# Performance work log

Hardware: AMD Instinct MI355X
Metric: run time of the kernel (lower is better)

The kernel has to match this reference:

```python
import jax, jax.numpy as jnp
import numpy as np

D_MODEL = 1024
N_HEAD = 16
DK = D_MODEL // N_HEAD
NEG = -10000.0  # module uses masked_fill with -10000.0, not -inf


def setup_inputs() -> dict:
    key = jax.random.key(0)
    k1, k2, k3 = jax.random.split(key, 3)
    B, T = 8, 1024
    x = jax.random.normal(k1, (B, T, D_MODEL), dtype=jnp.float32)
    # torch Linear(d, 3d, bias=False): y = x @ W.T with W [3d, d]; store transposed
    w_qkv = jax.random.normal(k2, (D_MODEL, 3 * D_MODEL), dtype=jnp.float32) * (1.0 / np.sqrt(D_MODEL))
    w_proj = jax.random.normal(k3, (D_MODEL, D_MODEL), dtype=jnp.float32) * (1.0 / np.sqrt(D_MODEL))
    return {"x": x, "w_qkv": w_qkv, "w_proj": w_proj}


def reference(x, w_qkv, w_proj):
    B, T, C = x.shape
    qkv = x @ w_qkv  # [B, T, 3C]
    q, k, v = jnp.split(qkv, 3, axis=-1)
    # [B, H, T, dk]
    q = q.reshape(B, T, N_HEAD, DK).transpose(0, 2, 1, 3)
    k = k.reshape(B, T, N_HEAD, DK).transpose(0, 2, 1, 3)
    v = v.reshape(B, T, N_HEAD, DK).transpose(0, 2, 1, 3)
    att = jnp.einsum('bhqd,bhkd->bhqk', q, k) / jnp.sqrt(jnp.float32(DK))
    causal = jnp.tril(jnp.ones((T, T), dtype=bool))  # [T, T]
    att = jnp.where(causal[None, None], att, NEG)
    att = jax.nn.softmax(att, axis=-1)
    y = jnp.einsum('bhqk,bhkd->bhqd', att, v)  # [B, H, T, dk]
    y = y.transpose(0, 2, 1, 3).reshape(B, T, C)
    return y @ w_proj
```

## Files before the change

kernel.cpp:

```cpp
#include <hip/hip_runtime.h>

typedef short bf16x8 __attribute__((ext_vector_type(8)));
typedef float f32x4 __attribute__((ext_vector_type(4)));
typedef unsigned u32x4 __attribute__((ext_vector_type(4)));

__device__ __forceinline__ unsigned short f2bf(float f) {
  unsigned u = __builtin_bit_cast(unsigned, f);
  u += 0x7fff + ((u >> 16) & 1);
  return (unsigned short)(u >> 16);
}

__device__ __forceinline__ void gload_lds16(const void* g, void* l) {
  __builtin_amdgcn_global_load_lds(
      (const __attribute__((address_space(1))) void*)g,
      (__attribute__((address_space(3))) void*)l, 16, 0, 0);
}

__global__ __launch_bounds__(256) void prep(const float* __restrict__ x,
                                            const float* __restrict__ wqkv,
                                            const float* __restrict__ wproj,
                                            unsigned short* __restrict__ xb,
                                            unsigned short* __restrict__ wqkvT,
                                            unsigned short* __restrict__ wprojT) {
  __shared__ float tile[32][33];
  const int tid = threadIdx.x;
  const int bid = blockIdx.x;
  if (bid < 2048) {
    int i = bid * 256 + tid;
    const int stride = 2048 * 256;
    for (; i < 2097152; i += stride) {
      float4 v = ((const float4*)x)[i];
      ushort4 o;
      o.x = f2bf(v.x); o.y = f2bf(v.y); o.z = f2bf(v.z); o.w = f2bf(v.w);
      ((ushort4*)xb)[i] = o;
    }
    return;
  }
  const float* in;
  unsigned short* out;
  int R, C, c0, r0;
  if (bid < 5120) {
    int b = bid - 2048;
    in = wqkv; out = wqkvT; R = 1024; C = 3072;
    c0 = (b % 96) * 32; r0 = (b / 96) * 32;
  } else {
    int b = bid - 5120;
    in = wproj; out = wprojT; R = 1024; C = 1024;
    c0 = (b % 32) * 32; r0 = (b / 32) * 32;
  }
  const int tr = tid >> 3;
  const int tc4 = tid & 7;
  float4 v = *(const float4*)&in[(size_t)(r0 + tr) * C + c0 + tc4 * 4];
  tile[tr][tc4 * 4 + 0] = v.x;
  tile[tr][tc4 * 4 + 1] = v.y;
  tile[tr][tc4 * 4 + 2] = v.z;
  tile[tr][tc4 * 4 + 3] = v.w;
  __syncthreads();
#pragma unroll
  for (int i = 0; i < 4; ++i)
    out[(size_t)(c0 + tr) * R + r0 + tc4 * 4 + i] = f2bf(tile[tc4 * 4 + i][tr]);
}

__global__ __launch_bounds__(256) void transpV(const unsigned short* __restrict__ qkv,
                                               unsigned short* __restrict__ vT) {
  const int tt = blockIdx.x, bh = blockIdx.y;
  const int b = bh >> 4, h = bh & 15;
  __shared__ unsigned short tile[64 * 64];
  const int tid = threadIdx.x;
  const size_t gbase = (size_t)b * 1024 * 3072 + 2048 + (size_t)h * 64;
#pragma unroll
  for (int i = 0; i < 2; ++i) {
    int c = i * 256 + tid;
    int trow = c >> 3, dc = c & 7;
    *(uint4*)(&tile[c * 8]) =
        *(const uint4*)(qkv + gbase + (size_t)(tt * 64 + trow) * 3072 + dc * 8);
  }
  __syncthreads();
  const int d = tid & 63, th = tid >> 6;
  unsigned short buf[16];
#pragma unroll
  for (int j = 0; j < 16; ++j) buf[j] = tile[(th * 16 + j) * 64 + d];
  size_t obase = ((size_t)bh * 64 + d) * 1024 + tt * 64 + th * 16;
  *(uint4*)(&vT[obase]) = *(uint4*)(&buf[0]);
  *(uint4*)(&vT[obase + 8]) = *(uint4*)(&buf[8]);
}

template <int OUT_BF16>
__global__ __launch_bounds__(256) void gemm_bt(const unsigned short* __restrict__ A,
                                               const unsigned short* __restrict__ B,
                                               void* __restrict__ Cv,
                                               int M, int N, int K, int lda) {
  __shared__ unsigned short As[128 * 64];
  __shared__ unsigned short Bs[128 * 64];
  const int tid = threadIdx.x;
  const int wv = tid >> 6, lane = tid & 63;
  const int l15 = lane & 15, lg = lane >> 4;
  const int bm = blockIdx.y, bn = blockIdx.x;
  const int wr = wv >> 1, wc = wv & 1;
  f32x4 acc[4][4] = {};
  const unsigned short* Ab = A + (size_t)bm * 128 * lda;
  const unsigned short* Bb = B + (size_t)bn * 128 * K;

  for (int k0 = 0; k0 < K; k0 += 64) {
#pragma unroll
    for (int i = 0; i < 4; ++i) {
      int s = i * 256 + wv * 64 + lane;
      int row = s >> 3, pc = s & 7;
      int lc = pc ^ (row & 7);
      gload_lds16(Ab + (size_t)row * lda + k0 + lc * 8,
                  (char*)As + (size_t)(i * 256 + wv * 64) * 16);
      gload_lds16(Bb + (size_t)row * K + k0 + lc * 8,
                  (char*)Bs + (size_t)(i * 256 + wv * 64) * 16);
    }
    __syncthreads();
#pragma unroll
    for (int kh = 0; kh < 2; ++kh) {
      bf16x8 af[4], bf[4];
#pragma unroll
      for (int m = 0; m < 4; ++m) {
        int row = wr * 64 + m * 16 + l15;
        int pc = (kh * 4 + lg) ^ (row & 7);
        af[m] = *(const bf16x8*)((const char*)As + (row * 8 + pc) * 16);
      }
#pragma unroll
      for (int n = 0; n < 4; ++n) {
        int row = wc * 64 + n * 16 + l15;
        int pc = (kh * 4 + lg) ^ (row & 7);
        bf[n] = *(const bf16x8*)((const char*)Bs + (row * 8 + pc) * 16);
      }
#pragma unroll
      for (int m = 0; m < 4; ++m)
#pragma unroll
        for (int n = 0; n < 4; ++n)
          acc[m][n] = __builtin_amdgcn_mfma_f32_16x16x32_bf16(af[m], bf[n], acc[m][n], 0, 0, 0);
    }
    __syncthreads();
  }

  const int rbase = bm * 128 + wr * 64;
  const int cbase = bn * 128 + wc * 64;
#pragma unroll
  for (int m = 0; m < 4; ++m)
#pragma unroll
    for (int n = 0; n < 4; ++n)
#pragma unroll
      for (int r = 0; r < 4; ++r) {
        int row = rbase + m * 16 + lg * 4 + r;
        int col = cbase + n * 16 + l15;
        float v = acc[m][n][r];
        if (OUT_BF16)
          ((unsigned short*)Cv)[(size_t)row * N + col] = f2bf(v);
        else
          ((float*)Cv)[(size_t)row * N + col] = v;
      }
}

__global__ __launch_bounds__(256) void attn_fwd(const unsigned short* __restrict__ qkv,
                                                const unsigned short* __restrict__ vT,
                                                unsigned short* __restrict__ qkv_y) {
  const int bh = blockIdx.x;
  const int pair = blockIdx.y;
  const int b = bh >> 4, h = bh & 15;
  const int tid = threadIdx.x;
  const int wv = tid >> 6, lane = tid & 63;
  const int l15 = lane & 15, lg = lane >> 4;

  __shared__ unsigned short Ks[2][64 * 64];
  __shared__ unsigned short Vs[2][64 * 64];

  const size_t base = (size_t)b * 1024 * 3072;
  const float CSCL = 0.18033688f;
  const int kq = wv * 16 + l15;

  const int idx0 = (l15 + ((lg & 1) << 5)) << 2;
  const int idx1 = idx0 + 64;
  const bool hi_nt = (lg & 2) != 0;

#pragma unroll
  for (int phase = 0; phase < 2; ++phase) {
    const int qt = phase ? 15 - pair : pair;
    const int q0 = qt * 64;
    const int qrow = q0 + wv * 16 + l15;
    const int rowg_base = q0 + wv * 16 + lg * 4;

    bf16x8 qa[2];
#pragma unroll
    for (int kh = 0; kh < 2; ++kh)
      qa[kh] = *(const bf16x8*)(qkv + base + (size_t)qrow * 3072 + h * 64 + kh * 32 + lg * 8);

    float l_sum = 0.f;
    f32x4 oacc[4] = {};

#pragma unroll
    for (int i = 0; i < 2; ++i) {
      int s = i * 256 + wv * 64 + lane;
      int row = s >> 3, pc = s & 7;
      int lc = pc ^ (row & 7);
      gload_lds16(qkv + base + (size_t)row * 3072 + 1024 + h * 64 + lc * 8,
                  (char*)(&Ks[0][0]) + (size_t)s * 16);
      gload_lds16(vT + ((size_t)bh * 64 + row) * 1024 + lc * 8,
                  (char*)(&Vs[0][0]) + (size_t)s * 16);
    }
    __syncthreads();

    for (int t = 0; t <= qt; ++t) {
      const int cur = t & 1;
      if (t < qt) {
        const int kv1 = (t + 1) * 64;
#pragma unroll
        for (int i = 0; i < 2; ++i) {
          int s = i * 256 + wv * 64 + lane;
          int row = s >> 3, pc = s & 7;
          int lc = pc ^ (row & 7);
          gload_lds16(qkv + base + (size_t)(kv1 + row) * 3072 + 1024 + h * 64 + lc * 8,
                      (char*)(&Ks[cur ^ 1][0]) + (size_t)s * 16);
          gload_lds16(vT + ((size_t)bh * 64 + row) * 1024 + kv1 + lc * 8,
                      (char*)(&Vs[cur ^ 1][0]) + (size_t)s * 16);
        }
      }

      f32x4 sacc[4] = {};
#pragma unroll
      for (int kh = 0; kh < 2; ++kh) {
        bf16x8 kf[4];
#pragma unroll
        for (int nt = 0; nt < 4; ++nt) {
          int row = nt * 16 + l15;
          int pc = (kh * 4 + lg) ^ (row & 7);
          kf[nt] = *(const bf16x8*)((const char*)(&Ks[cur][0]) + (row * 8 + pc) * 16);
        }
#pragma unroll
        for (int nt = 0; nt < 4; ++nt)
          sacc[nt] = __builtin_amdgcn_mfma_f32_16x16x32_bf16(kf[nt], qa[kh], sacc[nt], 0, 0, 0);
      }

      const bool diag = (t == qt);
      float sv[4][4];
#pragma unroll
      for (int nt = 0; nt < 4; ++nt)
#pragma unroll
        for (int r = 0; r < 4; ++r) {
          float s = sacc[nt][r] * CSCL;
          if (diag && (nt * 16 + lg * 4 + r > kq)) s = -1e30f;
          sv[nt][r] = exp2f(s);
        }

      {
        float ts = 0.f;
#pragma unroll
        for (int nt = 0; nt < 4; ++nt)
#pragma unroll
          for (int r = 0; r < 4; ++r) ts += sv[nt][r];
        ts += __shfl_xor(ts, 16);
        ts += __shfl_xor(ts, 32);
        l_sum += ts;
      }

      unsigned P2[4][2];
#pragma unroll
      for (int nt = 0; nt < 4; ++nt)
#pragma unroll
        for (int i = 0; i < 2; ++i)
          asm("v_cvt_pk_bf16_f32 %0, %1, %2"
              : "=v"(P2[nt][i]) : "v"(sv[nt][2 * i]), "v"(sv[nt][2 * i + 1]));

      u32x4 paw0, paw1;
#pragma unroll
      for (int w = 0; w < 4; ++w) {
        int idx = (w & 2) ? idx1 : idx0;
        int ri = w & 1;
        unsigned a0 = (unsigned)__builtin_amdgcn_ds_bpermute(idx, (int)P2[0][ri]);
        unsigned b0 = (unsigned)__builtin_amdgcn_ds_bpermute(idx, (int)P2[1][ri]);
        paw0[w] = hi_nt ? b0 : a0;
        unsigned a1 = (unsigned)__builtin_amdgcn_ds_bpermute(idx, (int)P2[2][ri]);
        unsigned b1 = (unsigned)__builtin_amdgcn_ds_bpermute(idx, (int)P2[3][ri]);
        paw1[w] = hi_nt ? b1 : a1;
      }
      bf16x8 pa[2];
      pa[0] = __builtin_bit_cast(bf16x8, paw0);
      pa[1] = __builtin_bit_cast(bf16x8, paw1);

#pragma unroll
      for (int kh = 0; kh < 2; ++kh)
#pragma unroll
        for (int nt = 0; nt < 4; ++nt) {
          int row = nt * 16 + l15;
          int pc = (kh * 4 + lg) ^ (row & 7);
          bf16x8 vf = *(const bf16x8*)((const char*)(&Vs[cur][0]) + (row * 8 + pc) * 16);
          oacc[nt] = __builtin_amdgcn_mfma_f32_16x16x32_bf16(pa[kh], vf, oacc[nt], 0, 0, 0);
        }
      __syncthreads();
    }

    float linv[4];
#pragma unroll
    for (int r = 0; r < 4; ++r) {
      int q = lg * 4 + r;
      float lv = __builtin_bit_cast(
          float, __builtin_amdgcn_ds_bpermute(q << 2, __builtin_bit_cast(int, l_sum)));
      linv[r] = 1.0f / lv;
    }

#pragma unroll
    for (int nt = 0; nt < 4; ++nt) {
#pragma unroll
      for (int r = 0; r < 4; ++r) {
        int row = rowg_base + r;
        int col = h * 64 + nt * 16 + l15;
        qkv_y[((size_t)b * 1024 + row) * 3072 + 2048 + col] = f2bf(oacc[nt][r] * linv[r]);
      }
    }
    __syncthreads();
  }
}

extern "C" void kernel_launch(void* const* d_in, const int* in_sizes, int n_in,
                              void* d_out, int out_size, void* d_ws, size_t ws_size,
                              hipStream_t stream) {
  const float* x = (const float*)d_in[0];
  const float* w_qkv = (const float*)d_in[1];
  const float* w_proj = (const float*)d_in[2];

  unsigned short* xb     = (unsigned short*)d_ws;
  unsigned short* vT     = (unsigned short*)d_ws;
  unsigned short* wqkvT  = (unsigned short*)((char*)d_ws + (16u << 20));
  unsigned short* wprojT = (unsigned short*)((char*)d_ws + (22u << 20));
  unsigned short* qkvb   = (unsigned short*)((char*)d_ws + (24u << 20));

  prep<<<6144, 256, 0, stream>>>(x, w_qkv, w_proj, xb, wqkvT, wprojT);

  gemm_bt<1><<<dim3(24, 64), 256, 0, stream>>>(xb, wqkvT, qkvb, 8192, 3072, 1024, 1024);

  transpV<<<dim3(16, 128), 256, 0, stream>>>(qkvb, vT);

  attn_fwd<<<dim3(128, 8), 256, 0, stream>>>(qkvb, vT, qkvb);

  gemm_bt<0><<<dim3(8, 64), 256, 0, stream>>>(qkvb + 2048, wprojT, d_out, 8192, 1024, 1024, 3072);
}
```

Measured before the change: 230.3 us.

## Triple-buffer GEMM K-tiles with async LDS loads and register prefetch

Replaces the single-buffered GEMM, which used a 64-wide K tile and two barriers per step, with a three-slot LDS ring of 32-wide K tiles. Global-to-LDS loads are issued ahead of use, and fragments for the next tile are read into registers while MFMAs run on the current one. There is now one barrier per step, plus manual waitcnt/sched_barrier control and setprio around the MFMA block. The aim is to hide global memory latency behind compute. In exchange the XOR swizzle is dropped, which may cause LDS bank conflicts, and each barrier now covers fewer MFMAs.

```diff
diff --git a/kernel.cpp b/kernel.cpp
--- a/kernel.cpp
+++ b/kernel.cpp
@@ -86,12 +86,12 @@
 }
 
 template <int OUT_BF16>
-__global__ __launch_bounds__(256) void gemm_bt(const unsigned short* __restrict__ A,
-                                               const unsigned short* __restrict__ B,
-                                               void* __restrict__ Cv,
-                                               int M, int N, int K, int lda) {
-  __shared__ unsigned short As[128 * 64];
-  __shared__ unsigned short Bs[128 * 64];
+__global__ __launch_bounds__(256, 3) void gemm_p3(const unsigned short* __restrict__ A,
+                                                  const unsigned short* __restrict__ B,
+                                                  void* __restrict__ Cv,
+                                                  int M, int N, int K, int lda) {
+  __shared__ unsigned short As[3][128 * 32];
+  __shared__ unsigned short Bs[3][128 * 32];
   const int tid = threadIdx.x;
   const int wv = tid >> 6, lane = tid & 63;
   const int l15 = lane & 15, lg = lane >> 4;
@@ -100,42 +100,66 @@
   f32x4 acc[4][4] = {};
   const unsigned short* Ab = A + (size_t)bm * 128 * lda;
   const unsigned short* Bb = B + (size_t)bn * 128 * K;
-
-  for (int k0 = 0; k0 < K; k0 += 64) {
-#pragma unroll
-    for (int i = 0; i < 4; ++i) {
+  const int NT = K >> 5;
+
+  auto STAGE = [&](int t) {
+    int slot = t % 3;
+#pragma unroll
+    for (int i = 0; i < 2; ++i) {
       int s = i * 256 + wv * 64 + lane;
-      int row = s >> 3, pc = s & 7;
-      int lc = pc ^ (row & 7);
-      gload_lds16(Ab + (size_t)row * lda + k0 + lc * 8,
-                  (char*)As + (size_t)(i * 256 + wv * 64) * 16);
-      gload_lds16(Bb + (size_t)row * K + k0 + lc * 8,
-                  (char*)Bs + (size_t)(i * 256 + wv * 64) * 16);
-    }
-    __syncthreads();
-#pragma unroll
-    for (int kh = 0; kh < 2; ++kh) {
-      bf16x8 af[4], bf[4];
-#pragma unroll
-      for (int m = 0; m < 4; ++m) {
-        int row = wr * 64 + m * 16 + l15;
-        int pc = (kh * 4 + lg) ^ (row & 7);
-        af[m] = *(const bf16x8*)((const char*)As + (row * 8 + pc) * 16);
-      }
-#pragma unroll
-      for (int n = 0; n < 4; ++n) {
-        int row = wc * 64 + n * 16 + l15;
-        int pc = (kh * 4 + lg) ^ (row & 7);
-        bf[n] = *(const bf16x8*)((const char*)Bs + (row * 8 + pc) * 16);
-      }
-#pragma unroll
-      for (int m = 0; m < 4; ++m)
-#pragma unroll
-        for (int n = 0; n < 4; ++n)
-          acc[m][n] = __builtin_amdgcn_mfma_f32_16x16x32_bf16(af[m], bf[n], acc[m][n], 0, 0, 0);
-    }
-    __syncthreads();
-  }
+      int row = s >> 2, cc = s & 3;
+      gload_lds16(Ab + (size_t)row * lda + t * 32 + cc * 8,
+                  (char*)(&As[slot][0]) + (size_t)(i * 256 + wv * 64) * 16);
+      gload_lds16(Bb + (size_t)row * K + t * 32 + cc * 8,
+                  (char*)(&Bs[slot][0]) + (size_t)(i * 256 + wv * 64) * 16);
+    }
+  };
+
+  bf16x8 af[4], bf[4];
+
+  STAGE(0); STAGE(1); STAGE(2);
+  asm volatile("s_waitcnt vmcnt(4)" ::: "memory");
+  __builtin_amdgcn_s_barrier();
+#pragma unroll
+  for (int m = 0; m < 4; ++m)
+    af[m] = *(const bf16x8*)(&As[0][0] + (wr * 64 + m * 16 + l15) * 32 + lg * 8);
+#pragma unroll
+  for (int n = 0; n < 4; ++n)
+    bf[n] = *(const bf16x8*)(&Bs[0][0] + (wc * 64 + n * 16 + l15) * 32 + lg * 8);
+  asm volatile("s_waitcnt lgkmcnt(0)" ::: "memory");
+  __builtin_amdgcn_sched_barrier(0);
+  __builtin_amdgcn_s_barrier();
+  __builtin_amdgcn_sched_barrier(0);
+
+  for (int t = 0; t < NT; ++t) {
+    __builtin_amdgcn_s_setprio(1);
+#pragma unroll
+    for (int m = 0; m < 4; ++m)
+#pragma unroll
+      for (int n = 0; n < 4; ++n)
+        acc[m][n] = __builtin_amdgcn_mfma_f32_16x16x32_bf16(af[m], bf[n], acc[m][n], 0, 0, 0);
+    __builtin_amdgcn_s_setprio(0);
+    if (t == NT - 1) break;
+
+    const unsigned short* as = &As[(t + 1) % 3][0];
+    const unsigned short* bs = &Bs[(t + 1) % 3][0];
+#pragma unroll
+    for (int m = 0; m < 4; ++m)
+      af[m] = *(const bf16x8*)(as + (wr * 64 + m * 16 + l15) * 32 + lg * 8);
+#pragma unroll
+    for (int n = 0; n < 4; ++n)
+      bf[n] = *(const bf16x8*)(bs + (wc * 64 + n * 16 + l15) * 32 + lg * 8);
+
+    STAGE(t + 3 < NT ? t + 3 : NT - 1);
+
+    asm volatile("s_waitcnt vmcnt(4)" ::: "memory");
+    asm volatile("s_waitcnt lgkmcnt(0)" ::: "memory");
+    __builtin_amdgcn_sched_barrier(0);
+    __builtin_amdgcn_s_barrier();
+    __builtin_amdgcn_sched_barrier(0);
+  }
+
+  asm volatile("s_waitcnt vmcnt(0)" ::: "memory");
 
   const int rbase = bm * 128 + wr * 64;
   const int cbase = bn * 128 + wc * 64;
@@ -329,11 +353,11 @@
 
   prep<<<6144, 256, 0, stream>>>(x, w_qkv, w_proj, xb, wqkvT, wprojT);
 
-  gemm_bt<1><<<dim3(24, 64), 256, 0, stream>>>(xb, wqkvT, qkvb, 8192, 3072, 1024, 1024);
+  gemm_p3<1><<<dim3(24, 64), 256, 0, stream>>>(xb, wqkvT, qkvb, 8192, 3072, 1024, 1024);
 
   transpV<<<dim3(16, 128), 256, 0, stream>>>(qkvb, vT);
 
   attn_fwd<<<dim3(128, 8), 256, 0, stream>>>(qkvb, vT, qkvb);
 
-  gemm_bt<0><<<dim3(8, 64), 256, 0, stream>>>(qkvb + 2048, wprojT, d_out, 8192, 1024, 1024, 3072);
-}
+  gemm_p3<0><<<dim3(8, 64), 256, 0, stream>>>(qkvb + 2048, wprojT, d_out, 8192, 1024, 1024, 3072);
+}
```

Result: slower. 239.3 us (+3.9%).

## Compute V transposed via swapped-operand GEMM and drop transpose kernel

Applied to the files above, without the earlier changes.

Splits the QKV projection into a Q/K GEMM and a separate GEMM that computes V already transposed by swapping operands. This removes the standalone V transpose kernel and its extra read and write of V. Attention addressing and workspace layout are updated, and the attention output now lives in a compact buffer for the output projection. It adds one more GEMM launch with a different tile shape.

```diff
diff --git a/kernel.cpp b/kernel.cpp
--- a/kernel.cpp
+++ b/kernel.cpp
@@ -61,30 +61,6 @@
     out[(size_t)(c0 + tr) * R + r0 + tc4 * 4 + i] = f2bf(tile[tc4 * 4 + i][tr]);
 }
 
-__global__ __launch_bounds__(256) void transpV(const unsigned short* __restrict__ qkv,
-                                               unsigned short* __restrict__ vT) {
-  const int tt = blockIdx.x, bh = blockIdx.y;
-  const int b = bh >> 4, h = bh & 15;
-  __shared__ unsigned short tile[64 * 64];
-  const int tid = threadIdx.x;
-  const size_t gbase = (size_t)b * 1024 * 3072 + 2048 + (size_t)h * 64;
-#pragma unroll
-  for (int i = 0; i < 2; ++i) {
-    int c = i * 256 + tid;
-    int trow = c >> 3, dc = c & 7;
-    *(uint4*)(&tile[c * 8]) =
-        *(const uint4*)(qkv + gbase + (size_t)(tt * 64 + trow) * 3072 + dc * 8);
-  }
-  __syncthreads();
-  const int d = tid & 63, th = tid >> 6;
-  unsigned short buf[16];
-#pragma unroll
-  for (int j = 0; j < 16; ++j) buf[j] = tile[(th * 16 + j) * 64 + d];
-  size_t obase = ((size_t)bh * 64 + d) * 1024 + tt * 64 + th * 16;
-  *(uint4*)(&vT[obase]) = *(uint4*)(&buf[0]);
-  *(uint4*)(&vT[obase + 8]) = *(uint4*)(&buf[8]);
-}
-
 template <int OUT_BF16>
 __global__ __launch_bounds__(256) void gemm_bt(const unsigned short* __restrict__ A,
                                                const unsigned short* __restrict__ B,
@@ -155,9 +131,9 @@
       }
 }
 
-__global__ __launch_bounds__(256) void attn_fwd(const unsigned short* __restrict__ qkv,
+__global__ __launch_bounds__(256) void attn_fwd(const unsigned short* __restrict__ qk2,
                                                 const unsigned short* __restrict__ vT,
-                                                unsigned short* __restrict__ qkv_y) {
+                                                unsigned short* __restrict__ yb) {
   const int bh = blockIdx.x;
   const int pair = blockIdx.y;
   const int b = bh >> 4, h = bh & 15;
@@ -168,7 +144,8 @@
   __shared__ unsigned short Ks[2][64 * 64];
   __shared__ unsigned short Vs[2][64 * 64];
 
-  const size_t base = (size_t)b * 1024 * 3072;
+  const size_t base = (size_t)b * 1024 * 2048;
+  const size_t vbase = (size_t)(h * 64) * 8192 + (size_t)b * 1024;
   const float CSCL = 0.18033688f;
   const int kq = wv * 16 + l15;
 
@@ -186,7 +163,7 @@
     bf16x8 qa[2];
 #pragma unroll
     for (int kh = 0; kh < 2; ++kh)
-      qa[kh] = *(const bf16x8*)(qkv + base + (size_t)qrow * 3072 + h * 64 + kh * 32 + lg * 8);
+      qa[kh] = *(const bf16x8*)(qk2 + base + (size_t)qrow * 2048 + h * 64 + kh * 32 + lg * 8);
 
     float l_sum = 0.f;
     f32x4 oacc[4] = {};
@@ -196,9 +173,9 @@
       int s = i * 256 + wv * 64 + lane;
       int row = s >> 3, pc = s & 7;
       int lc = pc ^ (row & 7);
-      gload_lds16(qkv + base + (size_t)row * 3072 + 1024 + h * 64 + lc * 8,
+      gload_lds16(qk2 + base + (size_t)row * 2048 + 1024 + h * 64 + lc * 8,
                   (char*)(&Ks[0][0]) + (size_t)s * 16);
-      gload_lds16(vT + ((size_t)bh * 64 + row) * 1024 + lc * 8,
+      gload_lds16(vT + vbase + (size_t)row * 8192 + lc * 8,
                   (char*)(&Vs[0][0]) + (size_t)s * 16);
     }
     __syncthreads();
@@ -212,9 +189,9 @@
           int s = i * 256 + wv * 64 + lane;
           int row = s >> 3, pc = s & 7;
           int lc = pc ^ (row & 7);
-          gload_lds16(qkv + base + (size_t)(kv1 + row) * 3072 + 1024 + h * 64 + lc * 8,
+          gload_lds16(qk2 + base + (size_t)(kv1 + row) * 2048 + 1024 + h * 64 + lc * 8,
                       (char*)(&Ks[cur ^ 1][0]) + (size_t)s * 16);
-          gload_lds16(vT + ((size_t)bh * 64 + row) * 1024 + kv1 + lc * 8,
+          gload_lds16(vT + vbase + (size_t)row * 8192 + kv1 + lc * 8,
                       (char*)(&Vs[cur ^ 1][0]) + (size_t)s * 16);
         }
       }
@@ -307,7 +284,7 @@
       for (int r = 0; r < 4; ++r) {
         int row = rowg_base + r;
         int col = h * 64 + nt * 16 + l15;
-        qkv_y[((size_t)b * 1024 + row) * 3072 + 2048 + col] = f2bf(oacc[nt][r] * linv[r]);
+        yb[((size_t)b * 1024 + row) * 1024 + col] = f2bf(oacc[nt][r] * linv[r]);
       }
     }
     __syncthreads();
@@ -322,18 +299,19 @@
   const float* w_proj = (const float*)d_in[2];
 
   unsigned short* xb     = (unsigned short*)d_ws;
-  unsigned short* vT     = (unsigned short*)d_ws;
+  unsigned short* yb     = (unsigned short*)d_ws;
   unsigned short* wqkvT  = (unsigned short*)((char*)d_ws + (16u << 20));
   unsigned short* wprojT = (unsigned short*)((char*)d_ws + (22u << 20));
-  unsigned short* qkvb   = (unsigned short*)((char*)d_ws + (24u << 20));
+  unsigned short* qk2    = (unsigned short*)((char*)d_ws + (24u << 20));
+  unsigned short* vT     = (unsigned short*)((char*)d_ws + (56u << 20));
 
   prep<<<6144, 256, 0, stream>>>(x, w_qkv, w_proj, xb, wqkvT, wprojT);
 
-  gemm_bt<1><<<dim3(24, 64), 256, 0, stream>>>(xb, wqkvT, qkvb, 8192, 3072, 1024, 1024);
-
-  transpV<<<dim3(16, 128), 256, 0, stream>>>(qkvb, vT);
-
-  attn_fwd<<<dim3(128, 8), 256, 0, stream>>>(qkvb, vT, qkvb);
-
-  gemm_bt<0><<<dim3(8, 64), 256, 0, stream>>>(qkvb + 2048, wprojT, d_out, 8192, 1024, 1024, 3072);
-}
+  gemm_bt<1><<<dim3(16, 64), 256, 0, stream>>>(xb, wqkvT, qk2, 8192, 2048, 1024, 1024);
+
+  gemm_bt<1><<<dim3(64, 8), 256, 0, stream>>>(wqkvT + 2048 * 1024, xb, vT, 1024, 8192, 1024, 1024);
+
+  attn_fwd<<<dim3(128, 8), 256, 0, stream>>>(qk2, vT, yb);
+
+  gemm_bt<0><<<dim3(8, 64), 256, 0, stream>>>(yb, wprojT, d_out, 8192, 1024, 1024, 1024);
+}
```

After: 228.0 us. No clear change (-1.0%).
